# Kernel optimization log

Measured on AMD Instinct MI355X. Metric: run time of the kernel, lower is better.

The kernel has to match this reference:

```python
import jax, jax.numpy as jnp
import numpy as np

D_IN = 4096
D_OUT = 4096
RANK = 16
ALPHA = 32
SCALE = ALPHA / RANK


def setup_inputs() -> dict:
    key = jax.random.key(0)
    k_x, k_w, k_b, k_a = jax.random.split(key, 4)
    x = jax.random.normal(k_x, (4, 2048, D_IN), dtype=jnp.float32)
    weight = jax.random.normal(k_w, (D_OUT, D_IN), dtype=jnp.float32) * (1.0 / np.sqrt(D_IN))
    bias = jax.random.normal(k_b, (D_OUT,), dtype=jnp.float32)
    lora_A = jax.random.normal(k_a, (RANK, D_IN), dtype=jnp.float32) * 0.01
    lora_B = jnp.zeros((D_OUT, RANK), dtype=jnp.float32)
    return {"x": x, "weight": weight, "bias": bias, "lora_A": lora_A, "lora_B": lora_B}


def reference(x, weight, bias, lora_A, lora_B):
    # base linear: y = x @ W^T + b   -> [B, S, D_OUT]
    orig_out = jnp.einsum("bsd,od->bso", x, weight) + bias
    # low-rank path: (x @ A^T) @ B^T * (alpha/rank)
    lora_out = jnp.einsum("bsr,or->bso", jnp.einsum("bsd,rd->bsr", x, lora_A), lora_B)
    return orig_out + lora_out * SCALE
```

## Files before the change

kernel.cpp:

```cpp
#include <hip/hip_runtime.h>
#include <stdint.h>

#define DIN   4096
#define DOUT  4096
#define RANK  16
#define MTOT  8192
#define LSCALE 2.0f

typedef unsigned short u16;
typedef __bf16 bf16x8 __attribute__((ext_vector_type(8)));
typedef float  f32x4  __attribute__((ext_vector_type(4)));
typedef u16    u16x8  __attribute__((ext_vector_type(8)));

__device__ __forceinline__ u16 f2bf(float f) {
    uint32_t u = __builtin_bit_cast(uint32_t, f);
    u = (u + 0x7FFFu + ((u >> 16) & 1u)) >> 16;
    return (u16)u;
}

__device__ __forceinline__ u16x8 pack8(f32x4 a, f32x4 b) {
    u16x8 o;
    o[0] = f2bf(a[0]); o[1] = f2bf(a[1]); o[2] = f2bf(a[2]); o[3] = f2bf(a[3]);
    o[4] = f2bf(b[0]); o[5] = f2bf(b[1]); o[6] = f2bf(b[2]); o[7] = f2bf(b[3]);
    return o;
}

#define GLDS16(g, l) __builtin_amdgcn_global_load_lds( \
    (const __attribute__((address_space(1))) void*)(g), \
    (__attribute__((address_space(3))) void*)(l), 16, 0, 0)

__global__ __launch_bounds__(256) void k_convert_x(const float* __restrict__ x,
                                                   u16* __restrict__ xb) {
    long i = ((long)blockIdx.x * 256 + threadIdx.x) * 8;
    f32x4 a = *(const f32x4*)(x + i);
    f32x4 b = *(const f32x4*)(x + i + 4);
    *(u16x8*)(xb + i) = pack8(a, b);
}

#define WEFF_OPG 16
__global__ __launch_bounds__(256) void k_build_weff(const float* __restrict__ W,
                                                    const float* __restrict__ A,
                                                    const float* __restrict__ B,
                                                    u16* __restrict__ wb) {
    const long t = (long)blockIdx.x * 256 + threadIdx.x;
    const int dc = (int)(t & 511);
    const int og = (int)(t >> 9);
    const int d  = dc * 8;
    f32x4 a0[RANK], a1[RANK];
#pragma unroll
    for (int r = 0; r < RANK; ++r) {
        a0[r] = *(const f32x4*)(A + (long)r * DIN + d);
        a1[r] = *(const f32x4*)(A + (long)r * DIN + d + 4);
    }
#pragma unroll 4
    for (int j = 0; j < WEFF_OPG; ++j) {
        const int o = og * WEFF_OPG + j;
        const long i = (long)o * DIN + d;
        f32x4 w0 = *(const f32x4*)(W + i);
        f32x4 w1 = *(const f32x4*)(W + i + 4);
#pragma unroll
        for (int r = 0; r < RANK; ++r) {
            const float s = B[o * RANK + r] * LSCALE;
            w0 += a0[r] * s;
            w1 += a1[r] * s;
        }
        *(u16x8*)(wb + i) = pack8(w0, w1);
    }
}

#define BM 256
#define BN 256
#define BK 64
#define NT (DIN / BK)

#define MFMA16(d, a, b) d = __builtin_amdgcn_mfma_f32_16x16x32_bf16(a, b, d, 0, 0, 0)
#define ABAR()   asm volatile("s_barrier" ::: "memory")
#define GATE4()  asm volatile("s_waitcnt vmcnt(4)" ::: "memory")
#define PRIO1()  __builtin_amdgcn_s_setprio(1)
#define PRIO0()  __builtin_amdgcn_s_setprio(0)

#define QUADK(mo, no, AF, BF) \
    _Pragma("unroll") \
    for (int kk = 0; kk < 2; ++kk) { \
        _Pragma("unroll") \
        for (int m = 0; m < 4; ++m) { \
            _Pragma("unroll") \
            for (int n = 0; n < 2; ++n) { \
                MFMA16(acc[(mo)+m][(no)+n], AF[m][kk], BF[n][kk]); \
            } \
        } \
    }

__global__ __launch_bounds__(512, 2) void k_gemm_ws(const u16* __restrict__ xb,
                                                    const u16* __restrict__ wb,
                                                    const float* __restrict__ bias,
                                                    float* __restrict__ out) {
    constexpr int K = DIN, N = DOUT;
    __shared__ alignas(16) u16 lds[65536];

    const int nchunk = gridDim.x >> 3;
    const int bid = blockIdx.x;
    const int wg  = (bid & 7) * nchunk + (bid >> 3);
    const int bm  = (wg & 31) * BM;
    const int bn  = (wg >> 5) * BN;

    const int tid  = threadIdx.x;
    const int lane = tid & 63;
    const int wid  = tid >> 6;
    const int wr   = wid >> 2;
    const int wc   = wid & 3;
    const int lrow = lane & 15;
    const int kgrp = lane >> 4;

    const int srow = tid >> 3;
    const int sgl  = (tid & 7) ^ (srow & 7);
    const u16* const aSrcB = xb + (long)(bm + srow) * K + sgl * 8;
    const u16* const bSrcB = wb + (long)(bn + srow) * K + sgl * 8;

#define STAGE_A(c, buf, kt) GLDS16(aSrcB + (long)(64*(c))*K + (kt)*BK, \
                                   lds + (buf)*16384 + (c)*4096 + tid*8)
#define STAGE_B(c, buf, kt) GLDS16(bSrcB + (long)(64*(c))*K + (kt)*BK, \
                                   lds + 32768 + (buf)*16384 + (c)*4096 + tid*8)

    const int go0 = (kgrp ^ (lrow & 7)) * 8;
    const int go1 = go0 ^ 32;
    const int arow = (wr*128 + lrow) * 64;
    const int brow = (wc*64  + lrow) * 64;

    const u16* const cA0 = lds +         arow;
    const u16* const cA1 = lds + 16384 + arow;
    const u16* const cB0 = lds + 32768 +         brow;
    const u16* const cB1 = lds + 32768 + 16384 + brow;

    f32x4 acc[8][4];
#pragma unroll
    for (int m = 0; m < 8; ++m)
#pragma unroll
        for (int n = 0; n < 4; ++n) acc[m][n] = (f32x4){0.f, 0.f, 0.f, 0.f};

    bf16x8 afL[4][2], afH[4][2], bfHi[2][2], bLoA[2][2], bLoB[2][2];

#define READ_AF(DST, BASE, OFS) \
    _Pragma("unroll") \
    for (int mf = 0; mf < 4; ++mf) { \
        const u16* b_ = (BASE) + ((OFS) + mf) * 1024; \
        DST[mf][0] = *(const bf16x8*)(b_ + go0); \
        DST[mf][1] = *(const bf16x8*)(b_ + go1); \
    }
#define READ_BF(DST, BASE, OFS) \
    _Pragma("unroll") \
    for (int nf = 0; nf < 2; ++nf) { \
        const u16* b_ = (BASE) + ((OFS) + nf) * 1024; \
        DST[nf][0] = *(const bf16x8*)(b_ + go0); \
        DST[nf][1] = *(const bf16x8*)(b_ + go1); \
    }

    STAGE_A(0, 0, 0); STAGE_A(1, 0, 0);
    STAGE_A(2, 0, 0); STAGE_A(3, 0, 0);
    STAGE_B(0, 0, 0); STAGE_B(1, 0, 0);
    STAGE_B(2, 0, 0); STAGE_B(3, 0, 0);
    STAGE_B(0, 1, 1); STAGE_B(1, 1, 1);
    STAGE_B(2, 1, 1); STAGE_B(3, 1, 1);
    GATE4();
    __syncthreads();
    READ_BF(bLoA, cB0, 0);

    for (int it = 0; it < NT/2; ++it) {
        const int kt1 = 2*it + 1;
        const int kt2 = (2*it + 2) & (NT - 1);
        const int kt3 = (2*it + 3) & (NT - 1);

        STAGE_A(0, 1, kt1); STAGE_A(1, 1, kt1);
        STAGE_A(2, 1, kt1); STAGE_A(3, 1, kt1);
        READ_AF(afL, cA0, 0);
        READ_BF(bfHi, cB0, 2);
        PRIO1(); QUADK(0, 0, afL, bLoA); QUADK(0, 2, afL, bfHi); PRIO0();
        ABAR();
        STAGE_B(0, 0, kt2); STAGE_B(1, 0, kt2);
        STAGE_B(2, 0, kt2); STAGE_B(3, 0, kt2);
        GATE4();
        READ_AF(afH, cA0, 4);
        READ_BF(bLoB, cB1, 0);
        PRIO1(); QUADK(4, 0, afH, bLoA); QUADK(4, 2, afH, bfHi); PRIO0();
        ABAR();

        STAGE_A(0, 0, kt2); STAGE_A(1, 0, kt2);
        STAGE_A(2, 0, kt2); STAGE_A(3, 0, kt2);
        READ_AF(afL, cA1, 0);
        READ_BF(bfHi, cB1, 2);
        PRIO1(); QUADK(0, 0, afL, bLoB); QUADK(0, 2, afL, bfHi); PRIO0();
        ABAR();

        STAGE_B(0, 1, kt3); STAGE_B(1, 1, kt3);
        STAGE_B(2, 1, kt3); STAGE_B(3, 1, kt3);
        GATE4();
        READ_AF(afH, cA1, 4);
        READ_BF(bLoA, cB0, 0);
        PRIO1(); QUADK(4, 0, afH, bLoB); QUADK(4, 2, afH, bfHi); PRIO0();
        ABAR();
    }
    asm volatile("s_waitcnt vmcnt(0)" ::: "memory");

    const int orow = bm + wr*128 + kgrp*4;
    const int ocol = bn + wc*64 + lrow;
#pragma unroll
    for (int n = 0; n < 4; ++n) {
        const int col = ocol + n*16;
        const float bj = bias[col];
#pragma unroll
        for (int m = 0; m < 8; ++m) {
            const int row = orow + m*16;
#pragma unroll
            for (int r = 0; r < 4; ++r)
                out[(long)(row + r) * N + col] = acc[m][n][r] + bj;
        }
    }
}

__global__ __launch_bounds__(64) void k_lora_T(const float* __restrict__ x,
                                               const float* __restrict__ A,
                                               float* __restrict__ T) {
    const int m = blockIdx.x;
    const int lane = threadIdx.x;
    const float* xr = x + (long)m * DIN;
    float acc[RANK];
#pragma unroll
    for (int r = 0; r < RANK; ++r) acc[r] = 0.f;
    for (int k = lane * 4; k < DIN; k += 64 * 4) {
        f32x4 xv = *(const f32x4*)(xr + k);
#pragma unroll
        for (int r = 0; r < RANK; ++r) {
            f32x4 av = *(const f32x4*)(A + (long)r * DIN + k);
            acc[r] += xv[0] * av[0] + xv[1] * av[1] + xv[2] * av[2] + xv[3] * av[3];
        }
    }
#pragma unroll
    for (int r = 0; r < RANK; ++r)
        for (int off = 32; off > 0; off >>= 1) acc[r] += __shfl_down(acc[r], off);
    if (lane == 0) {
#pragma unroll
        for (int r = 0; r < RANK; ++r) T[(long)m * RANK + r] = acc[r] * LSCALE;
    }
}

__global__ __launch_bounds__(256) void k_gemm_nows(const float* __restrict__ x,
                                                   const float* __restrict__ W,
                                                   const float* __restrict__ bias,
                                                   const float* __restrict__ T,
                                                   const float* __restrict__ lB,
                                                   float* __restrict__ out) {
    constexpr int FBM = 128, FBN = 128, FBK = 32, K = DIN, N = DOUT;
    __shared__ __align__(16) u16 As[FBM * FBK];
    __shared__ __align__(16) u16 Bs[FBN * FBK];

    const int tid = threadIdx.x;
    const int bm = blockIdx.y * FBM;
    const int bn = blockIdx.x * FBN;
    const int lane = tid & 63;
    const int wid  = tid >> 6;
    const int wr = wid >> 1, wc = wid & 1;
    const int lrow = lane & 15;
    const int kgrp = lane >> 4;

    const int c0 = tid, c1 = tid + 256;
    const float* aS0 = x + (long)(bm + (c0 >> 2)) * K + (c0 & 3) * 8;
    const float* aS1 = x + (long)(bm + (c1 >> 2)) * K + (c1 & 3) * 8;
    const float* bS0 = W + (long)(bn + (c0 >> 2)) * K + (c0 & 3) * 8;
    const float* bS1 = W + (long)(bn + (c1 >> 2)) * K + (c1 & 3) * 8;
    u16* aD0 = As + c0 * 8;  u16* aD1 = As + c1 * 8;
    u16* bD0 = Bs + c0 * 8;  u16* bD1 = Bs + c1 * 8;

    const u16* aR = As + (wr * 64 + lrow) * FBK + kgrp * 8;
    const u16* bR = Bs + (wc * 64 + lrow) * FBK + kgrp * 8;

    f32x4 acc[4][4];
#pragma unroll
    for (int i = 0; i < 4; ++i)
#pragma unroll
        for (int j = 0; j < 4; ++j) acc[i][j] = (f32x4){0.f, 0.f, 0.f, 0.f};

    for (int k0 = 0; k0 < K; k0 += FBK) {
        f32x4 a00 = *(const f32x4*)aS0, a01 = *(const f32x4*)(aS0 + 4);
        f32x4 a10 = *(const f32x4*)aS1, a11 = *(const f32x4*)(aS1 + 4);
        f32x4 b00 = *(const f32x4*)bS0, b01 = *(const f32x4*)(bS0 + 4);
        f32x4 b10 = *(const f32x4*)bS1, b11 = *(const f32x4*)(bS1 + 4);
        aS0 += FBK; aS1 += FBK; bS0 += FBK; bS1 += FBK;
        if (k0) __syncthreads();
        *(u16x8*)aD0 = pack8(a00, a01);
        *(u16x8*)aD1 = pack8(a10, a11);
        *(u16x8*)bD0 = pack8(b00, b01);
        *(u16x8*)bD1 = pack8(b10, b11);
        __syncthreads();

        bf16x8 af[4], bf[4];
#pragma unroll
        for (int i = 0; i < 4; ++i) af[i] = *(const bf16x8*)(aR + i * 16 * FBK);
#pragma unroll
        for (int j = 0; j < 4; ++j) bf[j] = *(const bf16x8*)(bR + j * 16 * FBK);
#pragma unroll
        for (int i = 0; i < 4; ++i)
#pragma unroll
            for (int j = 0; j < 4; ++j)
                acc[i][j] = __builtin_amdgcn_mfma_f32_16x16x32_bf16(af[i], bf[j], acc[i][j], 0, 0, 0);
    }

#pragma unroll
    for (int j = 0; j < 4; ++j) {
        const int col = bn + wc * 64 + j * 16 + lrow;
        const float bj = bias[col];
        float bl[RANK];
#pragma unroll
        for (int q = 0; q < RANK; ++q) bl[q] = lB[(long)col * RANK + q];
#pragma unroll
        for (int i = 0; i < 4; ++i) {
            const int row0 = bm + wr * 64 + i * 16 + kgrp * 4;
#pragma unroll
            for (int r = 0; r < 4; ++r) {
                const int row = row0 + r;
                const float* Trow = T + (long)row * RANK;
                float s = bj;
#pragma unroll
                for (int q = 0; q < RANK; ++q) s += Trow[q] * bl[q];
                out[(long)row * N + col] = acc[i][j][r] + s;
            }
        }
    }
}

extern "C" void kernel_launch(void* const* d_in, const int* in_sizes, int n_in,
                              void* d_out, int out_size, void* d_ws, size_t ws_size,
                              hipStream_t stream) {
    const float* x    = (const float*)d_in[0];
    const float* W    = (const float*)d_in[1];
    const float* bias = (const float*)d_in[2];
    const float* lA   = (const float*)d_in[3];
    const float* lB   = (const float*)d_in[4];
    float* out = (float*)d_out;

    const size_t xb_bytes = (size_t)MTOT * DIN * sizeof(u16);
    const size_t wb_bytes = (size_t)DOUT * DIN * sizeof(u16);

    if (ws_size >= xb_bytes + wb_bytes) {
        u16* xb = (u16*)d_ws;
        u16* wb = (u16*)((char*)d_ws + xb_bytes);
        k_convert_x <<<(int)((long)MTOT * DIN / 8 / 256), 256, 0, stream>>>(x, xb);
        k_build_weff<<<(DOUT / WEFF_OPG) * (DIN / 8) / 256, 256, 0, stream>>>(W, lA, lB, wb);
        k_gemm_ws   <<<(MTOT / BM) * (DOUT / BN), 512, 0, stream>>>(xb, wb, bias, out);
    } else {
        float* T = (float*)d_ws;
        k_lora_T   <<<MTOT, 64, 0, stream>>>(x, lA, T);
        k_gemm_nows<<<dim3(DOUT / 128, MTOT / 128), 256, 0, stream>>>(x, W, bias, T, lB, out);
    }
}
```

Measured before the change: 290.0 us.

## Use 4 waves per block with 128x128 per-wave tiles in bf16 GEMM

Halves the GEMM workgroup from 8 waves to 4 (launch bounds 256,1). Each wave now owns a 128x128 output tile with a 64-register-vector accumulator, and the global-to-LDS staging issues 8 chunks per thread instead of 4. The wait gate is raised to vmcnt(8) to match. The aim is more MFMA work per LDS fragment read and fewer waves contending for barriers, at the cost of much higher register pressure, one block per CU, and less latency hiding.

```diff
diff --git a/kernel.cpp b/kernel.cpp
--- a/kernel.cpp
+++ b/kernel.cpp
@@ -75,7 +75,7 @@
 
 #define MFMA16(d, a, b) d = __builtin_amdgcn_mfma_f32_16x16x32_bf16(a, b, d, 0, 0, 0)
 #define ABAR()   asm volatile("s_barrier" ::: "memory")
-#define GATE4()  asm volatile("s_waitcnt vmcnt(4)" ::: "memory")
+#define GATE8()  asm volatile("s_waitcnt vmcnt(8)" ::: "memory")
 #define PRIO1()  __builtin_amdgcn_s_setprio(1)
 #define PRIO0()  __builtin_amdgcn_s_setprio(0)
 
@@ -85,13 +85,13 @@
         _Pragma("unroll") \
         for (int m = 0; m < 4; ++m) { \
             _Pragma("unroll") \
-            for (int n = 0; n < 2; ++n) { \
+            for (int n = 0; n < 4; ++n) { \
                 MFMA16(acc[(mo)+m][(no)+n], AF[m][kk], BF[n][kk]); \
             } \
         } \
     }
 
-__global__ __launch_bounds__(512, 2) void k_gemm_ws(const u16* __restrict__ xb,
+__global__ __launch_bounds__(256, 1) void k_gemm_ws(const u16* __restrict__ xb,
                                                     const u16* __restrict__ wb,
                                                     const float* __restrict__ bias,
                                                     float* __restrict__ out) {
@@ -107,8 +107,8 @@
     const int tid  = threadIdx.x;
     const int lane = tid & 63;
     const int wid  = tid >> 6;
-    const int wr   = wid >> 2;
-    const int wc   = wid & 3;
+    const int wr   = wid >> 1;
+    const int wc   = wid & 1;
     const int lrow = lane & 15;
     const int kgrp = lane >> 4;
 
@@ -117,94 +117,87 @@
     const u16* const aSrcB = xb + (long)(bm + srow) * K + sgl * 8;
     const u16* const bSrcB = wb + (long)(bn + srow) * K + sgl * 8;
 
-#define STAGE_A(c, buf, kt) GLDS16(aSrcB + (long)(64*(c))*K + (kt)*BK, \
-                                   lds + (buf)*16384 + (c)*4096 + tid*8)
-#define STAGE_B(c, buf, kt) GLDS16(bSrcB + (long)(64*(c))*K + (kt)*BK, \
-                                   lds + 32768 + (buf)*16384 + (c)*4096 + tid*8)
+#define STAGE_A(c, buf, kt) GLDS16(aSrcB + (long)(32*(c))*K + (kt)*BK, \
+                                   lds + (buf)*16384 + (c)*2048 + tid*8)
+#define STAGE_B(c, buf, kt) GLDS16(bSrcB + (long)(32*(c))*K + (kt)*BK, \
+                                   lds + 32768 + (buf)*16384 + (c)*2048 + tid*8)
 
     const int go0 = (kgrp ^ (lrow & 7)) * 8;
     const int go1 = go0 ^ 32;
     const int arow = (wr*128 + lrow) * 64;
-    const int brow = (wc*64  + lrow) * 64;
+    const int brow = (wc*128 + lrow) * 64;
 
     const u16* const cA0 = lds +         arow;
     const u16* const cA1 = lds + 16384 + arow;
     const u16* const cB0 = lds + 32768 +         brow;
     const u16* const cB1 = lds + 32768 + 16384 + brow;
 
-    f32x4 acc[8][4];
+    f32x4 acc[8][8];
 #pragma unroll
     for (int m = 0; m < 8; ++m)
 #pragma unroll
-        for (int n = 0; n < 4; ++n) acc[m][n] = (f32x4){0.f, 0.f, 0.f, 0.f};
-
-    bf16x8 afL[4][2], afH[4][2], bfHi[2][2], bLoA[2][2], bLoB[2][2];
-
-#define READ_AF(DST, BASE, OFS) \
+        for (int n = 0; n < 8; ++n) acc[m][n] = (f32x4){0.f, 0.f, 0.f, 0.f};
+
+    bf16x8 afL[4][2], afH[4][2], bfHi[4][2], bLoE[4][2], bLoO[4][2];
+
+#define READ_F4(DST, BASE, OFS) \
     _Pragma("unroll") \
-    for (int mf = 0; mf < 4; ++mf) { \
-        const u16* b_ = (BASE) + ((OFS) + mf) * 1024; \
-        DST[mf][0] = *(const bf16x8*)(b_ + go0); \
-        DST[mf][1] = *(const bf16x8*)(b_ + go1); \
-    }
-#define READ_BF(DST, BASE, OFS) \
-    _Pragma("unroll") \
-    for (int nf = 0; nf < 2; ++nf) { \
-        const u16* b_ = (BASE) + ((OFS) + nf) * 1024; \
-        DST[nf][0] = *(const bf16x8*)(b_ + go0); \
-        DST[nf][1] = *(const bf16x8*)(b_ + go1); \
-    }
-
-    STAGE_A(0, 0, 0); STAGE_A(1, 0, 0);
-    STAGE_A(2, 0, 0); STAGE_A(3, 0, 0);
-    STAGE_B(0, 0, 0); STAGE_B(1, 0, 0);
-    STAGE_B(2, 0, 0); STAGE_B(3, 0, 0);
-    STAGE_B(0, 1, 1); STAGE_B(1, 1, 1);
-    STAGE_B(2, 1, 1); STAGE_B(3, 1, 1);
-    GATE4();
+    for (int f = 0; f < 4; ++f) { \
+        const u16* b_ = (BASE) + ((OFS) + f) * 1024; \
+        DST[f][0] = *(const bf16x8*)(b_ + go0); \
+        DST[f][1] = *(const bf16x8*)(b_ + go1); \
+    }
+
+#pragma unroll
+    for (int c = 0; c < 8; ++c) STAGE_A(c, 0, 0);
+#pragma unroll
+    for (int c = 0; c < 8; ++c) STAGE_B(c, 0, 0);
+#pragma unroll
+    for (int c = 0; c < 8; ++c) STAGE_B(c, 1, 1);
+    GATE8();
     __syncthreads();
-    READ_BF(bLoA, cB0, 0);
+    READ_F4(bLoE, cB0, 0);
 
     for (int it = 0; it < NT/2; ++it) {
         const int kt1 = 2*it + 1;
         const int kt2 = (2*it + 2) & (NT - 1);
         const int kt3 = (2*it + 3) & (NT - 1);
 
-        STAGE_A(0, 1, kt1); STAGE_A(1, 1, kt1);
-        STAGE_A(2, 1, kt1); STAGE_A(3, 1, kt1);
-        READ_AF(afL, cA0, 0);
-        READ_BF(bfHi, cB0, 2);
-        PRIO1(); QUADK(0, 0, afL, bLoA); QUADK(0, 2, afL, bfHi); PRIO0();
+#pragma unroll
+        for (int c = 0; c < 8; ++c) STAGE_A(c, 1, kt1);
+        READ_F4(afL, cA0, 0);
+        READ_F4(bfHi, cB0, 4);
+        PRIO1(); QUADK(0, 0, afL, bLoE); QUADK(0, 4, afL, bfHi); PRIO0();
         ABAR();
-        STAGE_B(0, 0, kt2); STAGE_B(1, 0, kt2);
-        STAGE_B(2, 0, kt2); STAGE_B(3, 0, kt2);
-        GATE4();
-        READ_AF(afH, cA0, 4);
-        READ_BF(bLoB, cB1, 0);
-        PRIO1(); QUADK(4, 0, afH, bLoA); QUADK(4, 2, afH, bfHi); PRIO0();
+#pragma unroll
+        for (int c = 0; c < 8; ++c) STAGE_B(c, 0, kt2);
+        GATE8();
+        READ_F4(afH, cA0, 4);
+        READ_F4(bLoO, cB1, 0);
+        PRIO1(); QUADK(4, 0, afH, bLoE); QUADK(4, 4, afH, bfHi); PRIO0();
         ABAR();
 
-        STAGE_A(0, 0, kt2); STAGE_A(1, 0, kt2);
-        STAGE_A(2, 0, kt2); STAGE_A(3, 0, kt2);
-        READ_AF(afL, cA1, 0);
-        READ_BF(bfHi, cB1, 2);
-        PRIO1(); QUADK(0, 0, afL, bLoB); QUADK(0, 2, afL, bfHi); PRIO0();
+#pragma unroll
+        for (int c = 0; c < 8; ++c) STAGE_A(c, 0, kt2);
+        READ_F4(afL, cA1, 0);
+        READ_F4(bfHi, cB1, 4);
+        PRIO1(); QUADK(0, 0, afL, bLoO); QUADK(0, 4, afL, bfHi); PRIO0();
         ABAR();
 
-        STAGE_B(0, 1, kt3); STAGE_B(1, 1, kt3);
-        STAGE_B(2, 1, kt3); STAGE_B(3, 1, kt3);
-        GATE4();
-        READ_AF(afH, cA1, 4);
-        READ_BF(bLoA, cB0, 0);
-        PRIO1(); QUADK(4, 0, afH, bLoB); QUADK(4, 2, afH, bfHi); PRIO0();
+#pragma unroll
+        for (int c = 0; c < 8; ++c) STAGE_B(c, 1, kt3);
+        GATE8();
+        READ_F4(afH, cA1, 4);
+        READ_F4(bLoE, cB0, 0);
+        PRIO1(); QUADK(4, 0, afH, bLoO); QUADK(4, 4, afH, bfHi); PRIO0();
         ABAR();
     }
     asm volatile("s_waitcnt vmcnt(0)" ::: "memory");
 
     const int orow = bm + wr*128 + kgrp*4;
-    const int ocol = bn + wc*64 + lrow;
-#pragma unroll
-    for (int n = 0; n < 4; ++n) {
+    const int ocol = bn + wc*128 + lrow;
+#pragma unroll
+    for (int n = 0; n < 8; ++n) {
         const int col = ocol + n*16;
         const float bj = bias[col];
 #pragma unroll
@@ -345,7 +338,7 @@
         u16* wb = (u16*)((char*)d_ws + xb_bytes);
         k_convert_x <<<(int)((long)MTOT * DIN / 8 / 256), 256, 0, stream>>>(x, xb);
         k_build_weff<<<(DOUT / WEFF_OPG) * (DIN / 8) / 256, 256, 0, stream>>>(W, lA, lB, wb);
-        k_gemm_ws   <<<(MTOT / BM) * (DOUT / BN), 512, 0, stream>>>(xb, wb, bias, out);
+        k_gemm_ws   <<<(MTOT / BM) * (DOUT / BN), 256, 0, stream>>>(xb, wb, bias, out);
     } else {
         float* T = (float*)d_ws;
         k_lora_T   <<<MTOT, 64, 0, stream>>>(x, lA, T);
```

Result: slower. 405.9 us (+40.0%).
